# Performance work log

Measured on AMD Instinct MI355X. Metric: run time of the kernel, lower is better.

## Reference

```python
import jax, jax.numpy as jnp
import numpy as np

N = 32768          # total nodes
B = 64             # graphs
NPG = N // B       # nodes per graph (equal-sized graphs)
E = 524288         # edges (before self-loops)
D_IN, HID, HEADS, D_OUT = 128, 64, 4, 128
DH = HID * HEADS   # 256
NEG_SLOPE = 0.2
EPS = 1e-5

def _leaky(x):
    return jnp.where(x >= 0, x, NEG_SLOPE * x)

def gat_conv(x, src, dst, W, a_src, a_dst, b, concat):
    """PyG-style GATConv (self-loops already included in src/dst)."""
    H, C = a_src.shape
    h = (x @ W).reshape(N, H, C)                       # [N,H,C]
    es = jnp.einsum('nhc,hc->nh', h, a_src)            # score from source feats
    ed = jnp.einsum('nhc,hc->nh', h, a_dst)            # score from target feats
    e = _leaky(es[src] + ed[dst])                      # [E',H]
    m = jax.ops.segment_max(e, dst, num_segments=N)    # stable softmax per dst
    p = jnp.exp(e - m[dst])
    s = jax.ops.segment_sum(p, dst, num_segments=N)
    alpha = p / s[dst]                                 # [E',H]
    out = jax.ops.segment_sum(h[src] * alpha[..., None], dst, num_segments=N)
    out = out.reshape(N, H * C) if concat else out.mean(axis=1)
    return out + b

def mha(x, Wi, bi, Wo, bo, heads):
    """torch.nn.MultiheadAttention (batch_first, no mask, eval)."""
    Bb, T, D = x.shape
    qkv = x @ Wi.T + bi                                # [B,T,3D]
    q, k, v = jnp.split(qkv, 3, axis=-1)
    hd = D // heads
    def sp(t):
        return t.reshape(Bb, T, heads, hd).transpose(0, 2, 1, 3)  # [B,h,T,hd]
    q, k, v = sp(q), sp(k), sp(v)
    scores = jnp.einsum('bhqd,bhkd->bhqk', q, k) / jnp.sqrt(jnp.float32(hd))
    attn = jax.nn.softmax(scores, axis=-1)
    o = jnp.einsum('bhqk,bhkd->bhqd', attn, v)
    o = o.transpose(0, 2, 1, 3).reshape(Bb, T, D)
    return o @ Wo.T + bo

def layer_norm(x, g, b):
    mu = x.mean(-1, keepdims=True)
    var = x.var(-1, keepdims=True)
    return (x - mu) / jnp.sqrt(var + EPS) * g + b

def setup_inputs() -> dict:
    key = jax.random.key(0)
    ks = jax.random.split(key, 20)
    s = 0.1
    inp = {
        'x': jax.random.normal(ks[0], (N, D_IN), jnp.float32),
        'edge_index': jax.random.randint(ks[1], (2, E), 0, N, jnp.int64),
        'batch': (jnp.arange(N, dtype=jnp.int64) // NPG),
        # gat1: D_IN -> HEADS*HID (concat)
        'W1': jax.random.normal(ks[2], (D_IN, HEADS * HID), jnp.float32) * s,
        'aS1': jax.random.normal(ks[3], (HEADS, HID), jnp.float32) * s,
        'aD1': jax.random.normal(ks[4], (HEADS, HID), jnp.float32) * s,
        'b1': jnp.zeros((HEADS * HID,), jnp.float32),
        # gat2: DH -> HEADS*HID (concat)
        'W2': jax.random.normal(ks[5], (DH, HEADS * HID), jnp.float32) * s,
        'aS2': jax.random.normal(ks[6], (HEADS, HID), jnp.float32) * s,
        'aD2': jax.random.normal(ks[7], (HEADS, HID), jnp.float32) * s,
        'b2': jnp.zeros((HEADS * HID,), jnp.float32),
        # gat3: DH -> D_OUT, heads=1, concat=False (mean)
        'W3': jax.random.normal(ks[8], (DH, D_OUT), jnp.float32) * s,
        'aS3': jax.random.normal(ks[9], (1, D_OUT), jnp.float32) * s,
        'aD3': jax.random.normal(ks[10], (1, D_OUT), jnp.float32) * s,
        'b3': jnp.zeros((D_OUT,), jnp.float32),
        # MultiheadAttention
        'Wi': jax.random.normal(ks[11], (3 * DH, DH), jnp.float32) * s,
        'bi': jnp.zeros((3 * DH,), jnp.float32),
        'Wo': jax.random.normal(ks[12], (DH, DH), jnp.float32) * s,
        'bo': jnp.zeros((DH,), jnp.float32),
        # LayerNorm
        'gamma': jnp.ones((DH,), jnp.float32),
        'beta': jnp.zeros((DH,), jnp.float32),
    }
    return inp

def reference(x, edge_index, batch, W1, aS1, aD1, b1, W2, aS2, aD2, b2,
              W3, aS3, aD3, b3, Wi, bi, Wo, bo, gamma, beta):
    # add self-loops (PyG GATConv default)
    loops = jnp.arange(N, dtype=edge_index.dtype)
    src = jnp.concatenate([edge_index[0], loops])
    dst = jnp.concatenate([edge_index[1], loops])

    x1 = jax.nn.elu(gat_conv(x, src, dst, W1, aS1, aD1, b1, concat=True))
    x2 = jax.nn.elu(gat_conv(x1, src, dst, W2, aS2, aD2, b2, concat=True))

    # ragged-to-dense batching: batch = arange(N)//NPG (equal-sized, sorted),
    # so the torch python loop reduces to a reshape with no padding.
    x2b = x2.reshape(B, NPG, DH)
    attended = mha(x2b, Wi, bi, Wo, bo, HEADS).reshape(N, DH)

    x2a = layer_norm(attended + x2, gamma, beta)
    x3 = gat_conv(x2a, src, dst, W3, aS3, aD3, b3, concat=False)
    return x3
```

## Files before the change

### kernel.cpp

```cpp
#include <hip/hip_runtime.h>

typedef _Float16 half_t;
typedef _Float16 half8  __attribute__((ext_vector_type(8)));
typedef _Float16 half4v __attribute__((ext_vector_type(4)));
typedef float    f32x4  __attribute__((ext_vector_type(4)));

constexpr int N_NODES = 32768;
constexpr int NPG_    = 512;

#define MFMA16(a, b, c) __builtin_amdgcn_mfma_f32_16x16x32_f16((a), (b), (c), 0, 0, 0)

__device__ __forceinline__ void gload_lds16(const half_t* g, half_t* l) {
  __builtin_amdgcn_global_load_lds(
      (const __attribute__((address_space(1))) void*)g,
      (__attribute__((address_space(3))) void*)l, 16, 0, 0);
}

__global__ void k_hist(const int* __restrict__ dst, int* __restrict__ deg, int E) {
  int i = blockIdx.x * 256 + threadIdx.x;
  if (i < E) atomicAdd(&deg[dst[i]], 1);
}

__global__ __launch_bounds__(1024) void k_scan(const int* __restrict__ deg,
                                               int* __restrict__ rowptr) {
  __shared__ int part[1024];
  int t = threadIdx.x;
  int base = t * 32;
  int s = 0;
  #pragma unroll
  for (int i = 0; i < 32; i++) s += deg[base + i];
  part[t] = s;
  __syncthreads();
  for (int off = 1; off < 1024; off <<= 1) {
    int add = (t >= off) ? part[t - off] : 0;
    __syncthreads();
    part[t] += add;
    __syncthreads();
  }
  int run = (t == 0) ? 0 : part[t - 1];
  for (int i = 0; i < 32; i++) { rowptr[base + i] = run; run += deg[base + i]; }
  if (t == 1023) rowptr[N_NODES] = run;
}

__global__ void k_selfloop(const int* __restrict__ rowptr, int* __restrict__ fill,
                           int* __restrict__ col) {
  int i = blockIdx.x * 256 + threadIdx.x;
  fill[i] = 1;
  col[rowptr[i]] = i;
}

__global__ void k_scatter(const int* __restrict__ src, const int* __restrict__ dst,
                          const int* __restrict__ rowptr, int* __restrict__ fill,
                          int* __restrict__ col, int E) {
  int i = blockIdx.x * 256 + threadIdx.x;
  if (i < E) {
    int d = dst[i];
    int pos = rowptr[d] + atomicAdd(&fill[d], 1);
    col[pos] = src[i];
  }
}

__global__ void k_convert(
    const float* __restrict__ x,  half_t* __restrict__ x_h,
    const float* __restrict__ W1, half_t* __restrict__ W1t,
    const float* __restrict__ W2, half_t* __restrict__ W2t,
    const float* __restrict__ W3, half_t* __restrict__ W3t,
    const float* __restrict__ Wi, half_t* __restrict__ Wi_h,
    const float* __restrict__ Wo, half_t* __restrict__ Wo_h,
    int* __restrict__ deg)
{
  int bid = blockIdx.x, t = threadIdx.x;
  if (bid < 16384) {
    int i = bid * 256 + t;
    x_h[i] = (half_t)x[i];
  } else if (bid < 16512) {
    int i = (bid - 16384) * 256 + t;
    int o = i >> 7, k = i & 127;
    W1t[i] = (half_t)W1[k * 256 + o];
  } else if (bid < 16768) {
    int i = (bid - 16512) * 256 + t;
    int o = i >> 8, k = i & 255;
    W2t[i] = (half_t)W2[k * 256 + o];
  } else if (bid < 16896) {
    int i = (bid - 16768) * 256 + t;
    int o = i >> 8, k = i & 255;
    W3t[i] = (half_t)W3[k * 128 + o];
  } else if (bid < 17664) {
    int i = (bid - 16896) * 256 + t;
    Wi_h[i] = (half_t)Wi[i];
  } else if (bid < 17920) {
    int i = (bid - 17664) * 256 + t;
    Wo_h[i] = (half_t)Wo[i];
  } else {
    deg[(bid - 17920) * 256 + t] = 1;
  }
}

__global__ __launch_bounds__(256) void k_gemm(
    const half_t* __restrict__ A, const half_t* __restrict__ Bt,
    const float* __restrict__ bias, int bias_per_row,
    half_t* __restrict__ outh, float* __restrict__ outf,
    int M, int Nc, int K,
    const float* __restrict__ aS, const float* __restrict__ aD,
    float* __restrict__ es, float* __restrict__ ed, int H)
{
  __shared__ __align__(16) half_t As[128 * 64];
  __shared__ __align__(16) half_t Bs[128 * 64];
  __shared__ float sRed[2][4][64];
  int w = threadIdx.x >> 6, lane = threadIdx.x & 63;
  int r = lane & 15, q = lane >> 4;
  int m0 = blockIdx.y * 128, n0 = blockIdx.x * 128;
  int mh = (w & 1) * 64, nh = (w >> 1) * 64;
  f32x4 acc[4][4];
  #pragma unroll
  for (int i = 0; i < 4; i++)
    #pragma unroll
    for (int j = 0; j < 4; j++) acc[i][j] = f32x4{0.f, 0.f, 0.f, 0.f};

  int srow = lane >> 3;
  int sc   = lane & 7;

  for (int k0 = 0; k0 < K; k0 += 64) {
    __syncthreads();
    #pragma unroll
    for (int i = 0; i < 4; i++) {
      int R0 = w * 32 + i * 8;
      int row = R0 + srow;
      int cg = sc ^ (row & 7);
      gload_lds16(A  + (size_t)(m0 + row) * K + k0 + cg * 8, &As[R0 * 64]);
      gload_lds16(Bt + (size_t)(n0 + row) * K + k0 + cg * 8, &Bs[R0 * 64]);
    }
    __syncthreads();
    #pragma unroll
    for (int kk = 0; kk < 2; kk++) {
      half8 af[4], bf[4];
      #pragma unroll
      for (int t = 0; t < 4; t++) {
        int rr = mh + t * 16 + r;
        af[t] = *(const half8*)&As[rr * 64 + (((kk * 4 + q) ^ (rr & 7)) << 3)];
      }
      #pragma unroll
      for (int t = 0; t < 4; t++) {
        int rr = nh + t * 16 + r;
        bf[t] = *(const half8*)&Bs[rr * 64 + (((kk * 4 + q) ^ (rr & 7)) << 3)];
      }
      #pragma unroll
      for (int ti = 0; ti < 4; ti++)
        #pragma unroll
        for (int tj = 0; tj < 4; tj++)
          acc[ti][tj] = MFMA16(af[ti], bf[tj], acc[ti][tj]);
    }
  }

  #pragma unroll
  for (int tj = 0; tj < 4; tj++) {
    int colc = n0 + nh + tj * 16 + r;
    #pragma unroll
    for (int ti = 0; ti < 4; ti++) {
      #pragma unroll
      for (int i = 0; i < 4; i++) {
        int row = m0 + mh + ti * 16 + q * 4 + i;
        float bv = bias ? (bias_per_row ? bias[row] : bias[colc]) : 0.f;
        float v = acc[ti][tj][i] + bv;
        size_t idx = (size_t)row * Nc + colc;
        if (outf) outf[idx] = v;
        if (outh) outh[idx] = (half_t)v;
      }
    }
  }

  if (es) {
    if (H == 4) {
      int head = (n0 >> 6) + (nh >> 6);
      float aSv[4], aDv[4];
      #pragma unroll
      for (int tj = 0; tj < 4; tj++) {
        int cl = tj * 16 + r;
        aSv[tj] = aS[head * 64 + cl];
        aDv[tj] = aD[head * 64 + cl];
      }
      #pragma unroll
      for (int ti = 0; ti < 4; ti++) {
        #pragma unroll
        for (int i = 0; i < 4; i++) {
          float ps = 0.f, pd = 0.f;
          #pragma unroll
          for (int tj = 0; tj < 4; tj++) {
            float av = acc[ti][tj][i];
            ps += av * aSv[tj];
            pd += av * aDv[tj];
          }
          #pragma unroll
          for (int off = 1; off < 16; off <<= 1) {
            ps += __shfl_xor(ps, off);
            pd += __shfl_xor(pd, off);
          }
          if (r == 0) {
            int row = m0 + mh + ti * 16 + q * 4 + i;
            es[(size_t)row * 4 + head] = ps;
            ed[(size_t)row * 4 + head] = pd;
          }
        }
      }
    } else {
      float aSv[4], aDv[4];
      #pragma unroll
      for (int tj = 0; tj < 4; tj++) {
        int c = nh + tj * 16 + r;
        aSv[tj] = aS[c];
        aDv[tj] = aD[c];
      }
      #pragma unroll
      for (int ti = 0; ti < 4; ti++) {
        #pragma unroll
        for (int i = 0; i < 4; i++) {
          float ps = 0.f, pd = 0.f;
          #pragma unroll
          for (int tj = 0; tj < 4; tj++) {
            float av = acc[ti][tj][i];
            ps += av * aSv[tj];
            pd += av * aDv[tj];
          }
          #pragma unroll
          for (int off = 1; off < 16; off <<= 1) {
            ps += __shfl_xor(ps, off);
            pd += __shfl_xor(pd, off);
          }
          if (r == 0) {
            int ri = ti * 16 + q * 4 + i;
            sRed[0][w][ri] = ps;
            sRed[1][w][ri] = pd;
          }
        }
      }
      __syncthreads();
      if (threadIdx.x < 128) {
        int row = threadIdx.x;
        int wlo = row >> 6, ri = row & 63;
        es[m0 + row] = sRed[0][wlo][ri] + sRed[0][wlo + 2][ri];
        ed[m0 + row] = sRed[1][wlo][ri] + sRed[1][wlo + 2][ri];
      }
    }
  }
}

__global__ __launch_bounds__(256) void k_gemm_ln(
    const half_t* __restrict__ A, const half_t* __restrict__ Bt,
    const float* __restrict__ bias, const half_t* __restrict__ res,
    const float* __restrict__ gamma, const float* __restrict__ beta,
    half_t* __restrict__ outh)
{
  __shared__ __align__(16) half_t As[64 * 64];
  __shared__ __align__(16) half_t Bs[256 * 64];
  __shared__ float sSum[4][64], sSq[4][64];
  __shared__ float sMR[64][2];
  int w = threadIdx.x >> 6, lane = threadIdx.x & 63;
  int r = lane & 15, q = lane >> 4;
  int m0 = blockIdx.x * 64;
  int nh = w * 64;
  f32x4 acc[4][4];
  #pragma unroll
  for (int i = 0; i < 4; i++)
    #pragma unroll
    for (int j = 0; j < 4; j++) acc[i][j] = f32x4{0.f, 0.f, 0.f, 0.f};

  int srow = lane >> 3, sc = lane & 7;

  for (int k0 = 0; k0 < 256; k0 += 64) {
    __syncthreads();
    #pragma unroll
    for (int i = 0; i < 2; i++) {
      int R0 = w * 16 + i * 8;
      int row = R0 + srow;
      int cg = sc ^ (row & 7);
      gload_lds16(A + (size_t)(m0 + row) * 256 + k0 + cg * 8, &As[R0 * 64]);
    }
    #pragma unroll
    for (int i = 0; i < 8; i++) {
      int R0 = w * 64 + i * 8;
      int row = R0 + srow;
      int cg = sc ^ (row & 7);
      gload_lds16(Bt + (size_t)row * 256 + k0 + cg * 8, &Bs[R0 * 64]);
    }
    __syncthreads();
    #pragma unroll
    for (int kk = 0; kk < 2; kk++) {
      half8 af[4], bf[4];
      #pragma unroll
      for (int t = 0; t < 4; t++) {
        int rr = t * 16 + r;
        af[t] = *(const half8*)&As[rr * 64 + (((kk * 4 + q) ^ (rr & 7)) << 3)];
      }
      #pragma unroll
      for (int t = 0; t < 4; t++) {
        int rr = nh + t * 16 + r;
        bf[t] = *(const half8*)&Bs[rr * 64 + (((kk * 4 + q) ^ (rr & 7)) << 3)];
      }
      #pragma unroll
      for (int ti = 0; ti < 4; ti++)
        #pragma unroll
        for (int tj = 0; tj < 4; tj++)
          acc[ti][tj] = MFMA16(af[ti], bf[tj], acc[ti][tj]);
    }
  }

  float gv[4], bv[4];
  #pragma unroll
  for (int tj = 0; tj < 4; tj++) {
    int col = nh + tj * 16 + r;
    gv[tj] = gamma[col];
    bv[tj] = beta[col];
  }
  #pragma unroll
  for (int ti = 0; ti < 4; ti++) {
    #pragma unroll
    for (int i = 0; i < 4; i++) {
      int row = ti * 16 + q * 4 + i;
      float s = 0.f, ss = 0.f;
      #pragma unroll
      for (int tj = 0; tj < 4; tj++) {
        int col = nh + tj * 16 + r;
        float v = acc[ti][tj][i] + bias[col]
                + (float)res[(size_t)(m0 + row) * 256 + col];
        acc[ti][tj][i] = v;
        s += v;
        ss += v * v;
      }
      #pragma unroll
      for (int off = 1; off < 16; off <<= 1) {
        s  += __shfl_xor(s, off);
        ss += __shfl_xor(ss, off);
      }
      if (r == 0) { sSum[w][row] = s; sSq[w][row] = ss; }
    }
  }
  __syncthreads();
  if (threadIdx.x < 64) {
    int row = threadIdx.x;
    float s  = sSum[0][row] + sSum[1][row] + sSum[2][row] + sSum[3][row];
    float ss = sSq[0][row] + sSq[1][row] + sSq[2][row] + sSq[3][row];
    float mean = s * (1.f / 256.f);
    float var  = ss * (1.f / 256.f) - mean * mean;
    sMR[row][0] = mean;
    sMR[row][1] = rsqrtf(var + 1e-5f);
  }
  __syncthreads();
  #pragma unroll
  for (int ti = 0; ti < 4; ti++) {
    #pragma unroll
    for (int i = 0; i < 4; i++) {
      int row = ti * 16 + q * 4 + i;
      float mean = sMR[row][0], rstd = sMR[row][1];
      #pragma unroll
      for (int tj = 0; tj < 4; tj++) {
        int col = nh + tj * 16 + r;
        outh[(size_t)(m0 + row) * 256 + col] =
            (half_t)((acc[ti][tj][i] - mean) * rstd * gv[tj] + bv[tj]);
      }
    }
  }
}

template<int HC, int H, bool FP16ACC>
__global__ __launch_bounds__(256) void k_agg(
    const half_t* __restrict__ h, const float* __restrict__ es,
    const float* __restrict__ ed, const float* __restrict__ bias,
    const int* __restrict__ rowptr, const int* __restrict__ col, int elu,
    float* __restrict__ outf, half_t* __restrict__ outh)
{
  constexpr int VPT = HC / 16;
  constexpr int NV8 = VPT / 8;
  constexpr int C = HC / H;
  int lane = threadIdx.x & 63;
  int g = lane >> 4, li = lane & 15;
  int n = blockIdx.x * 4 + (threadIdx.x >> 6);
  int cbase = li * VPT;
  int hl = cbase / C;
  float edn = ed[(size_t)n * H + hl];
  int j0 = rowptr[n], j1 = rowptr[n + 1];
  const half_t* hb = h + cbase;

  float sum0 = 0.f, sum1 = 0.f;

  if constexpr (FP16ACC) {
    half8 acc0[NV8], acc1[NV8];
    #pragma unroll
    for (int i = 0; i < NV8; i++) {
      acc0[i] = half8{0, 0, 0, 0, 0, 0, 0, 0};
      acc1[i] = half8{0, 0, 0, 0, 0, 0, 0, 0};
    }
    for (int j = j0 + g; j < j1; j += 8) {
      int jb = j + 4;
      int s0 = col[j];
      int s1 = col[(jb < j1) ? jb : j];
      float e0 = es[(size_t)s0 * H + hl] + edn;
      e0 = fmaxf(e0, 0.2f * e0);
      float e1 = es[(size_t)s1 * H + hl] + edn;
      e1 = fmaxf(e1, 0.2f * e1);
      e1 = (jb < j1) ? e1 : -1e30f;
      const half_t* hp0 = hb + (size_t)s0 * HC;
      const half_t* hp1 = hb + (size_t)s1 * HC;
      float p0 = exp2f(e0 * 1.44269504f - 8.65617025f);
      float p1 = exp2f(e1 * 1.44269504f - 8.65617025f);
      sum0 += p0; sum1 += p1;
      half_t q0 = (half_t)p0, q1 = (half_t)p1;
      half8 pv0 = {q0, q0, q0, q0, q0, q0, q0, q0};
      half8 pv1 = {q1, q1, q1, q1, q1, q1, q1, q1};
      #pragma unroll
      for (int i = 0; i < NV8; i++) {
        half8 v0 = *(const half8*)(hp0 + i * 8);
        half8 v1 = *(const half8*)(hp1 + i * 8);
        acc0[i] += pv0 * v0;
        acc1[i] += pv1 * v1;
      }
    }
    float sum = sum0 + sum1;
    sum += __shfl_xor(sum, 16);
    sum += __shfl_xor(sum, 32);
    float av[VPT];
    #pragma unroll
    for (int i = 0; i < VPT; i++) {
      av[i] = (float)acc0[i >> 3][i & 7] + (float)acc1[i >> 3][i & 7];
      av[i] += __shfl_xor(av[i], 16);
      av[i] += __shfl_xor(av[i], 32);
    }
    float inv = 1.f / sum;
    float v[VPT];
    #pragma unroll
    for (int i = 0; i < VPT; i++) {
      float t = av[i] * inv + bias[cbase + i];
      if (elu) t = (t > 0.f) ? t : __expf(t) - 1.f;
      v[i] = t;
    }
    if (g == 0) {
      size_t obase = (size_t)n * HC + cbase;
      if (outh) {
        #pragma unroll
        for (int p8 = 0; p8 < NV8; p8++) {
          half8 hv;
          #pragma unroll
          for (int i = 0; i < 8; i++) hv[i] = (half_t)v[p8 * 8 + i];
          *(half8*)(outh + obase + p8 * 8) = hv;
        }
      }
      if (outf) {
        #pragma unroll
        for (int p4 = 0; p4 < VPT / 4; p4++) {
          float4 fv = {v[p4 * 4], v[p4 * 4 + 1], v[p4 * 4 + 2], v[p4 * 4 + 3]};
          *(float4*)(outf + obase + p4 * 4) = fv;
        }
      }
    }
  } else {
    float acc0[VPT], acc1[VPT];
    #pragma unroll
    for (int i = 0; i < VPT; i++) { acc0[i] = 0.f; acc1[i] = 0.f; }
    for (int j = j0 + g; j < j1; j += 8) {
      int jb = j + 4;
      int s0 = col[j];
      int s1 = col[(jb < j1) ? jb : j];
      float e0 = es[(size_t)s0 * H + hl] + edn;
      e0 = fmaxf(e0, 0.2f * e0);
      float e1 = es[(size_t)s1 * H + hl] + edn;
      e1 = fmaxf(e1, 0.2f * e1);
      e1 = (jb < j1) ? e1 : -1e30f;
      const half_t* hp0 = hb + (size_t)s0 * HC;
      const half_t* hp1 = hb + (size_t)s1 * HC;
      float p0 = __expf(e0), p1 = __expf(e1);
      sum0 += p0; sum1 += p1;
      #pragma unroll
      for (int c8 = 0; c8 < NV8; c8++) {
        half8 a0 = *(const half8*)(hp0 + c8 * 8);
        half8 a1 = *(const half8*)(hp1 + c8 * 8);
        #pragma unroll
        for (int i = 0; i < 8; i++) {
          acc0[c8 * 8 + i] += p0 * (float)a0[i];
          acc1[c8 * 8 + i] += p1 * (float)a1[i];
        }
      }
    }
    float sum = sum0 + sum1;
    sum += __shfl_xor(sum, 16);
    sum += __shfl_xor(sum, 32);
    float av[VPT];
    #pragma unroll
    for (int i = 0; i < VPT; i++) {
      av[i] = acc0[i] + acc1[i];
      av[i] += __shfl_xor(av[i], 16);
      av[i] += __shfl_xor(av[i], 32);
    }
    float inv = 1.f / sum;
    float v[VPT];
    #pragma unroll
    for (int i = 0; i < VPT; i++) {
      float t = av[i] * inv + bias[cbase + i];
      if (elu) t = (t > 0.f) ? t : __expf(t) - 1.f;
      v[i] = t;
    }
    if (g == 0) {
      size_t obase = (size_t)n * HC + cbase;
      if (outh) {
        #pragma unroll
        for (int p8 = 0; p8 < NV8; p8++) {
          half8 hv;
          #pragma unroll
          for (int i = 0; i < 8; i++) hv[i] = (half_t)v[p8 * 8 + i];
          *(half8*)(outh + obase + p8 * 8) = hv;
        }
      }
      if (outf) {
        #pragma unroll
        for (int p4 = 0; p4 < VPT / 4; p4++) {
          float4 fv = {v[p4 * 4], v[p4 * 4 + 1], v[p4 * 4 + 2], v[p4 * 4 + 3]};
          *(float4*)(outf + obase + p4 * 4) = fv;
        }
      }
    }
  }
}

__global__ __launch_bounds__(256) void k_attn(
    const half_t* __restrict__ qk, const half_t* __restrict__ vt,
    half_t* __restrict__ o)
{
  __shared__ __align__(16) half_t Kt[128 * 64];
  __shared__ __align__(16) half_t Vt[64 * 128];
  __shared__ __align__(16) half_t Pb[4][16][136];

  int pair = blockIdx.x;
  int b = pair >> 2, hh = pair & 3;
  int q0 = blockIdx.y * 256;
  int w = threadIdx.x >> 6, lane = threadIdx.x & 63;
  int cc = lane & 15, qq = lane >> 4;
  int qb = q0 + w * 64;

  half8 qa0[4], qa1[4];
  #pragma unroll
  for (int qs = 0; qs < 4; qs++) {
    const half_t* Qp = qk + ((size_t)(b * NPG_ + qb + qs * 16 + cc) * 512 + hh * 64);
    qa0[qs] = *(const half8*)(Qp + qq * 8);
    qa1[qs] = *(const half8*)(Qp + 32 + qq * 8);
  }

  f32x4 oacc[4][4];
  #pragma unroll
  for (int a = 0; a < 4; a++)
    #pragma unroll
    for (int t = 0; t < 4; t++) oacc[a][t] = f32x4{0.f, 0.f, 0.f, 0.f};
  float rs[4] = {0.f, 0.f, 0.f, 0.f};

  const half_t* kb = qk + ((size_t)(b * NPG_) * 512 + 256 + hh * 64);
  const half_t* vb = vt + ((size_t)(hh * 64) * 32768 + b * NPG_);

  int krow_l = lane >> 3, ks_l = lane & 7;
  int vrow_l = lane >> 4, vs_l = lane & 15;

  for (int kt = 0; kt < 4; kt++) {
    __syncthreads();
    #pragma unroll
    for (int i = 0; i < 4; i++) {
      int R = (i * 4 + w) * 8;
      int kr = R + krow_l;
      gload_lds16(kb + (size_t)(kt * 128 + kr) * 512 + ((ks_l ^ (kr & 7)) * 8),
                  &Kt[R * 64]);
    }
    #pragma unroll
    for (int i = 0; i < 4; i++) {
      int D0 = (i * 4 + w) * 4;
      int d = D0 + vrow_l;
      gload_lds16(vb + (size_t)d * 32768 + kt * 128 + ((vs_l ^ (d & 15)) * 8),
                  &Vt[D0 * 128]);
    }
    __syncthreads();

    #pragma unroll
    for (int qs = 0; qs < 4; qs++) {
      #pragma unroll
      for (int mt = 0; mt < 8; mt++) {
        int key = mt * 16 + cc;
        half8 k0 = *(const half8*)&Kt[key * 64 + ((qq ^ (key & 7)) << 3)];
        half8 k1 = *(const half8*)&Kt[key * 64 + (((qq + 4) ^ (key & 7)) << 3)];
        f32x4 s = f32x4{0.f, 0.f, 0.f, 0.f};
        s = MFMA16(k0, qa0[qs], s);
        s = MFMA16(k1, qa1[qs], s);
        half4v ph;
        #pragma unroll
        for (int i = 0; i < 4; i++) {
          float p = exp2f(s[i] * 0.180336886f - 11.54156033f);
          rs[qs] += p;
          ph[i] = (half_t)p;
        }
        *(half4v*)&Pb[w][cc][mt * 16 + qq * 4] = ph;
      }
      #pragma unroll
      for (int kc = 0; kc < 4; kc++) {
        half8 a = *(const half8*)&Pb[w][cc][kc * 32 + qq * 8];
        #pragma unroll
        for (int nt = 0; nt < 4; nt++) {
          int d = nt * 16 + cc;
          half8 bb = *(const half8*)&Vt[d * 128 + (((kc * 4 + qq) ^ (d & 15)) << 3)];
          oacc[qs][nt] = MFMA16(a, bb, oacc[qs][nt]);
        }
      }
    }
  }

  #pragma unroll
  for (int qs = 0; qs < 4; qs++) {
    float r = rs[qs];
    r += __shfl_xor(r, 16);
    r += __shfl_xor(r, 32);
    #pragma unroll
    for (int i = 0; i < 4; i++) {
      float rsv = __shfl(r, qq * 4 + i);
      float inv = 1.f / rsv;
      int node = b * NPG_ + qb + qs * 16 + qq * 4 + i;
      #pragma unroll
      for (int nt = 0; nt < 4; nt++)
        o[(size_t)node * 256 + hh * 64 + nt * 16 + cc] = (half_t)(oacc[qs][nt][i] * inv);
    }
  }
}

extern "C" void kernel_launch(void* const* d_in, const int* in_sizes, int n_in,
                              void* d_out, int out_size, void* d_ws, size_t ws_size,
                              hipStream_t stream)
{
  const float* x    = (const float*)d_in[0];
  const int*   ei   = (const int*)d_in[1];
  const float* W1   = (const float*)d_in[3];
  const float* aS1  = (const float*)d_in[4];
  const float* aD1  = (const float*)d_in[5];
  const float* b1   = (const float*)d_in[6];
  const float* W2   = (const float*)d_in[7];
  const float* aS2  = (const float*)d_in[8];
  const float* aD2  = (const float*)d_in[9];
  const float* b2   = (const float*)d_in[10];
  const float* W3   = (const float*)d_in[11];
  const float* aS3  = (const float*)d_in[12];
  const float* aD3  = (const float*)d_in[13];
  const float* b3   = (const float*)d_in[14];
  const float* Wi   = (const float*)d_in[15];
  const float* bi   = (const float*)d_in[16];
  const float* Wo   = (const float*)d_in[17];
  const float* bo   = (const float*)d_in[18];
  const float* gam  = (const float*)d_in[19];
  const float* bet  = (const float*)d_in[20];
  float* out = (float*)d_out;
  const int N = N_NODES;
  int E = in_sizes[1] / 2;

  char* ws = (char*)d_ws;
  size_t off = 0;
  auto alloc = [&](size_t bytes) -> void* {
    void* p = ws + off;
    off = (off + bytes + 255) & ~(size_t)255;
    return p;
  };
  half_t* x_h    = (half_t*)alloc((size_t)N * 128 * 2);
  half_t* h_h    = (half_t*)alloc((size_t)N * 256 * 2);
  half_t* x1_h   = (half_t*)alloc((size_t)N * 256 * 2);
  half_t* x2_h   = (half_t*)alloc((size_t)N * 256 * 2);
  half_t* qk_h   = (half_t*)alloc((size_t)N * 512 * 2);
  half_t* vt_h   = (half_t*)alloc((size_t)256 * N * 2);
  half_t* o_h    = (half_t*)alloc((size_t)N * 256 * 2);
  half_t* x2a_h  = (half_t*)alloc((size_t)N * 256 * 2);
  half_t* W1t    = (half_t*)alloc(256 * 128 * 2);
  half_t* W2t    = (half_t*)alloc(256 * 256 * 2);
  half_t* W3t    = (half_t*)alloc(128 * 256 * 2);
  half_t* Wi_h   = (half_t*)alloc(768 * 256 * 2);
  half_t* Wo_h   = (half_t*)alloc(256 * 256 * 2);
  float*  es     = (float*) alloc((size_t)N * 4 * 4);
  float*  ed     = (float*) alloc((size_t)N * 4 * 4);
  int*    deg    = (int*)   alloc((size_t)N * 4);
  int*    fill   = (int*)   alloc((size_t)N * 4);
  int*    rowptr = (int*)   alloc(((size_t)N + 1) * 4);
  int*    col    = (int*)   alloc((size_t)(N + E) * 4);

  const int* srcE = ei;
  const int* dstE = ei + E;

  k_convert<<<18048, 256, 0, stream>>>(x, x_h, W1, W1t, W2, W2t, W3, W3t,
                                       Wi, Wi_h, Wo, Wo_h, deg);
  k_hist<<<(E + 255) / 256, 256, 0, stream>>>(dstE, deg, E);
  k_scan<<<1, 1024, 0, stream>>>(deg, rowptr);
  k_selfloop<<<N / 256, 256, 0, stream>>>(rowptr, fill, col);
  k_scatter<<<(E + 255) / 256, 256, 0, stream>>>(srcE, dstE, rowptr, fill, col, E);

  k_gemm<<<dim3(2, N / 128), 256, 0, stream>>>(x_h, W1t, nullptr, 0, h_h, nullptr,
                                               N, 256, 128, aS1, aD1, es, ed, 4);
  k_agg<256, 4, true><<<N / 4, 256, 0, stream>>>(h_h, es, ed, b1, rowptr, col, 1, nullptr, x1_h);

  k_gemm<<<dim3(2, N / 128), 256, 0, stream>>>(x1_h, W2t, nullptr, 0, h_h, nullptr,
                                               N, 256, 256, aS2, aD2, es, ed, 4);
  k_agg<256, 4, true><<<N / 4, 256, 0, stream>>>(h_h, es, ed, b2, rowptr, col, 1, nullptr, x2_h);

  k_gemm<<<dim3(4, N / 128), 256, 0, stream>>>(x2_h, Wi_h, bi, 0, qk_h, nullptr,
                                               N, 512, 256, nullptr, nullptr, nullptr, nullptr, 0);
  k_gemm<<<dim3(N / 128, 2), 256, 0, stream>>>(Wi_h + 512 * 256, x2_h, bi + 512, 1,
                                               vt_h, nullptr, 256, N, 256,
                                               nullptr, nullptr, nullptr, nullptr, 0);
  k_attn<<<dim3(256, 2), 256, 0, stream>>>(qk_h, vt_h, o_h);

  k_gemm_ln<<<N / 64, 256, 0, stream>>>(o_h, Wo_h, bo, x2_h, gam, bet, x2a_h);

  k_gemm<<<dim3(1, N / 128), 256, 0, stream>>>(x2a_h, W3t, nullptr, 0, h_h, nullptr,
                                               N, 128, 256, aS3, aD3, es, ed, 1);
  k_agg<128, 1, false><<<N / 4, 256, 0, stream>>>(h_h, es, ed, b3, rowptr, col, 0, out, nullptr);
}
```

Baseline: 448.3 us.

## Shrink attention tiles to 64 queries per block and 64-key chunks

The attention kernel now gives each wave 16 queries instead of 64 and streams keys and values in 64-wide chunks over 8 iterations instead of 128-wide over 4. The grid grows from 512 to 2048 blocks with smaller LDS and register footprints, which raises occupancy and fills more CUs. In exchange, K and V tiles are reloaded four times as often per head, and there are more barriers per unit of compute.

Result: no change. 446.1 us (-0.5%).

```diff
diff --git a/kernel.cpp b/kernel.cpp
--- a/kernel.cpp
+++ b/kernel.cpp
@@ -523,102 +523,83 @@
     const half_t* __restrict__ qk, const half_t* __restrict__ vt,
     half_t* __restrict__ o)
 {
-  __shared__ __align__(16) half_t Kt[128 * 64];
-  __shared__ __align__(16) half_t Vt[64 * 128];
-  __shared__ __align__(16) half_t Pb[4][16][136];
+  __shared__ __align__(16) half_t Kt[64 * 64];
+  __shared__ __align__(16) half_t Vt[64 * 64];
+  __shared__ __align__(16) half_t Pb[4][16][72];
 
   int pair = blockIdx.x;
   int b = pair >> 2, hh = pair & 3;
-  int q0 = blockIdx.y * 256;
+  int q0 = blockIdx.y * 64;
   int w = threadIdx.x >> 6, lane = threadIdx.x & 63;
   int cc = lane & 15, qq = lane >> 4;
-  int qb = q0 + w * 64;
-
-  half8 qa0[4], qa1[4];
-  #pragma unroll
-  for (int qs = 0; qs < 4; qs++) {
-    const half_t* Qp = qk + ((size_t)(b * NPG_ + qb + qs * 16 + cc) * 512 + hh * 64);
-    qa0[qs] = *(const half8*)(Qp + qq * 8);
-    qa1[qs] = *(const half8*)(Qp + 32 + qq * 8);
-  }
-
-  f32x4 oacc[4][4];
-  #pragma unroll
-  for (int a = 0; a < 4; a++)
-    #pragma unroll
-    for (int t = 0; t < 4; t++) oacc[a][t] = f32x4{0.f, 0.f, 0.f, 0.f};
-  float rs[4] = {0.f, 0.f, 0.f, 0.f};
+
+  const half_t* Qp = qk + ((size_t)(b * NPG_ + q0 + w * 16 + cc) * 512 + hh * 64);
+  half8 qa0 = *(const half8*)(Qp + qq * 8);
+  half8 qa1 = *(const half8*)(Qp + 32 + qq * 8);
+
+  f32x4 oacc[4];
+  #pragma unroll
+  for (int t = 0; t < 4; t++) oacc[t] = f32x4{0.f, 0.f, 0.f, 0.f};
+  float rs = 0.f;
 
   const half_t* kb = qk + ((size_t)(b * NPG_) * 512 + 256 + hh * 64);
   const half_t* vb = vt + ((size_t)(hh * 64) * 32768 + b * NPG_);
 
-  int krow_l = lane >> 3, ks_l = lane & 7;
-  int vrow_l = lane >> 4, vs_l = lane & 15;
-
-  for (int kt = 0; kt < 4; kt++) {
-    __syncthreads();
-    #pragma unroll
-    for (int i = 0; i < 4; i++) {
-      int R = (i * 4 + w) * 8;
-      int kr = R + krow_l;
-      gload_lds16(kb + (size_t)(kt * 128 + kr) * 512 + ((ks_l ^ (kr & 7)) * 8),
+  int krow = lane >> 3, ksl = lane & 7;
+
+  for (int kt = 0; kt < 8; kt++) {
+    __syncthreads();
+    #pragma unroll
+    for (int i = 0; i < 2; i++) {
+      int R = w * 16 + i * 8;
+      int kr = R + krow;
+      gload_lds16(kb + (size_t)(kt * 64 + kr) * 512 + ((ksl ^ (kr & 7)) * 8),
                   &Kt[R * 64]);
-    }
-    #pragma unroll
-    for (int i = 0; i < 4; i++) {
-      int D0 = (i * 4 + w) * 4;
-      int d = D0 + vrow_l;
-      gload_lds16(vb + (size_t)d * 32768 + kt * 128 + ((vs_l ^ (d & 15)) * 8),
-                  &Vt[D0 * 128]);
-    }
-    __syncthreads();
-
-    #pragma unroll
-    for (int qs = 0; qs < 4; qs++) {
-      #pragma unroll
-      for (int mt = 0; mt < 8; mt++) {
-        int key = mt * 16 + cc;
-        half8 k0 = *(const half8*)&Kt[key * 64 + ((qq ^ (key & 7)) << 3)];
-        half8 k1 = *(const half8*)&Kt[key * 64 + (((qq + 4) ^ (key & 7)) << 3)];
-        f32x4 s = f32x4{0.f, 0.f, 0.f, 0.f};
-        s = MFMA16(k0, qa0[qs], s);
-        s = MFMA16(k1, qa1[qs], s);
-        half4v ph;
-        #pragma unroll
-        for (int i = 0; i < 4; i++) {
-          float p = exp2f(s[i] * 0.180336886f - 11.54156033f);
-          rs[qs] += p;
-          ph[i] = (half_t)p;
-        }
-        *(half4v*)&Pb[w][cc][mt * 16 + qq * 4] = ph;
-      }
-      #pragma unroll
-      for (int kc = 0; kc < 4; kc++) {
-        half8 a = *(const half8*)&Pb[w][cc][kc * 32 + qq * 8];
-        #pragma unroll
-        for (int nt = 0; nt < 4; nt++) {
-          int d = nt * 16 + cc;
-          half8 bb = *(const half8*)&Vt[d * 128 + (((kc * 4 + qq) ^ (d & 15)) << 3)];
-          oacc[qs][nt] = MFMA16(a, bb, oacc[qs][nt]);
-        }
-      }
-    }
-  }
-
-  #pragma unroll
-  for (int qs = 0; qs < 4; qs++) {
-    float r = rs[qs];
-    r += __shfl_xor(r, 16);
-    r += __shfl_xor(r, 32);
-    #pragma unroll
-    for (int i = 0; i < 4; i++) {
-      float rsv = __shfl(r, qq * 4 + i);
-      float inv = 1.f / rsv;
-      int node = b * NPG_ + qb + qs * 16 + qq * 4 + i;
-      #pragma unroll
-      for (int nt = 0; nt < 4; nt++)
-        o[(size_t)node * 256 + hh * 64 + nt * 16 + cc] = (half_t)(oacc[qs][nt][i] * inv);
-    }
+      gload_lds16(vb + (size_t)kr * 32768 + kt * 64 + ((ksl ^ (kr & 7)) * 8),
+                  &Vt[R * 64]);
+    }
+    __syncthreads();
+
+    #pragma unroll
+    for (int mt = 0; mt < 4; mt++) {
+      int key = mt * 16 + cc;
+      half8 k0 = *(const half8*)&Kt[key * 64 + ((qq ^ (key & 7)) << 3)];
+      half8 k1 = *(const half8*)&Kt[key * 64 + (((qq + 4) ^ (key & 7)) << 3)];
+      f32x4 s = f32x4{0.f, 0.f, 0.f, 0.f};
+      s = MFMA16(k0, qa0, s);
+      s = MFMA16(k1, qa1, s);
+      half4v ph;
+      #pragma unroll
+      for (int i = 0; i < 4; i++) {
+        float p = exp2f(s[i] * 0.180336886f - 11.54156033f);
+        rs += p;
+        ph[i] = (half_t)p;
+      }
+      *(half4v*)&Pb[w][cc][mt * 16 + qq * 4] = ph;
+    }
+
+    #pragma unroll
+    for (int kc = 0; kc < 2; kc++) {
+      half8 a = *(const half8*)&Pb[w][cc][kc * 32 + qq * 8];
+      #pragma unroll
+      for (int nt = 0; nt < 4; nt++) {
+        int d = nt * 16 + cc;
+        half8 bb = *(const half8*)&Vt[d * 64 + (((kc * 4 + qq) ^ (d & 7)) << 3)];
+        oacc[nt] = MFMA16(a, bb, oacc[nt]);
+      }
+    }
+  }
+
+  rs += __shfl_xor(rs, 16);
+  rs += __shfl_xor(rs, 32);
+  #pragma unroll
+  for (int i = 0; i < 4; i++) {
+    float rsv = __shfl(rs, qq * 4 + i);
+    float inv = 1.f / rsv;
+    int node = b * NPG_ + q0 + w * 16 + qq * 4 + i;
+    #pragma unroll
+    for (int nt = 0; nt < 4; nt++)
+      o[(size_t)node * 256 + hh * 64 + nt * 16 + cc] = (half_t)(oacc[nt][i] * inv);
   }
 }
 
@@ -700,7 +681,7 @@
   k_gemm<<<dim3(N / 128, 2), 256, 0, stream>>>(Wi_h + 512 * 256, x2_h, bi + 512, 1,
                                                vt_h, nullptr, 256, N, 256,
                                                nullptr, nullptr, nullptr, nullptr, 0);
-  k_attn<<<dim3(256, 2), 256, 0, stream>>>(qk_h, vt_h, o_h);
+  k_attn<<<dim3(256, 8), 256, 0, stream>>>(qk_h, vt_h, o_h);
 
   k_gemm_ln<<<N / 64, 256, 0, stream>>>(o_h, Wo_h, bo, x2_h, gam, bet, x2a_h);
 
```
